# Kernel optimization log

Hardware: AMD Instinct MI355X
Metric: run time of the kernel (lower is better)

## Reference

```python
import jax, jax.numpy as jnp
import numpy as np

MAX_SCALE_MUL = float(np.log(100.0))
EPS = 1e-12

def _l2norm(t):
    # F.normalize(dim=-1): x / max(||x||_2, eps)
    n = jnp.sqrt(jnp.sum(t * t, axis=-1, keepdims=True))
    return t / jnp.maximum(n, EPS)

def setup_inputs() -> dict:
    key = jax.random.key(0)
    ks = jax.random.split(key, 6)
    B, L, C, H = 2, 2048, 1024, 16
    x = jax.random.normal(ks[0], (B, L, C), dtype=jnp.float32)
    attn_bias = jax.random.normal(ks[1], (1, 1, L, L), dtype=jnp.float32) * 0.02
    W_qkv = jax.random.normal(ks[2], (3 * C, C), dtype=jnp.float32) * (1.0 / np.sqrt(C))
    q_bias = jnp.zeros((C,), dtype=jnp.float32)
    v_bias = jnp.zeros((C,), dtype=jnp.float32)
    scale_mul_1H11 = jnp.full((1, H, 1, 1), np.log(4.0), dtype=jnp.float32)
    W_proj = jax.random.normal(ks[3], (C, C), dtype=jnp.float32) * (1.0 / np.sqrt(C))
    b_proj = jnp.zeros((C,), dtype=jnp.float32)
    return {"x": x, "attn_bias": attn_bias, "W_qkv": W_qkv, "q_bias": q_bias,
            "v_bias": v_bias, "scale_mul_1H11": scale_mul_1H11,
            "W_proj": W_proj, "b_proj": b_proj}

def reference(x, attn_bias, W_qkv, q_bias, v_bias, scale_mul_1H11, W_proj, b_proj):
    B, L, C = x.shape
    H = scale_mul_1H11.shape[1]
    D = C // H
    # qkv projection (no linear bias) + concatenated (q_bias, 0, v_bias)
    bias = jnp.concatenate([q_bias, jnp.zeros_like(q_bias), v_bias])
    pre_qkv = jnp.einsum('blc,oc->blo', x, W_qkv) + bias  # (B,L,3C)
    qkv = pre_qkv.reshape(B, L, 3, H, D).transpose(2, 0, 3, 1, 4)  # (3,B,H,L,D)
    q, k, v = qkv[0], qkv[1], qkv[2]
    # cosine attention: l2-normalize q,k; q scaled by learned per-head scale
    scale_mul = jnp.exp(jnp.minimum(scale_mul_1H11, MAX_SCALE_MUL))
    q = _l2norm(q) * scale_mul
    k = _l2norm(k)
    # slow_attn_original with scale=1 (attn_l2_norm path)
    attn = jnp.einsum('bhld,bhmd->bhlm', q, k) + attn_bias  # (B,H,L,L)
    attn = jax.nn.softmax(attn, axis=-1)
    oup = jnp.einsum('bhlm,bhmd->bhld', attn, v)  # (B,H,L,D)
    oup = oup.transpose(0, 2, 1, 3).reshape(B, L, C)
    return jnp.einsum('blc,oc->blo', oup, W_proj) + b_proj
```

## Files before the change

kernel.cpp:

```cpp
#include <hip/hip_runtime.h>

typedef short bf16x8 __attribute__((ext_vector_type(8)));
typedef short bf16x4 __attribute__((ext_vector_type(4)));
typedef unsigned short u16x8 __attribute__((ext_vector_type(8)));
typedef float f32x4 __attribute__((ext_vector_type(4)));

__device__ __forceinline__ float bf2f(unsigned short u) {
  union { unsigned int i; float f; } v; v.i = ((unsigned int)u) << 16; return v.f;
}
__device__ __forceinline__ unsigned short f2bf(float f) {
  union { float fl; unsigned int i; } v; v.fl = f;
  unsigned int r = v.i + 0x7FFFu + ((v.i >> 16) & 1u);
  return (unsigned short)(r >> 16);
}
__device__ __forceinline__ unsigned int cvt_pk_bf16(float lo, float hi) {
  unsigned int d;
  asm("v_cvt_pk_bf16_f32 %0, %1, %2" : "=v"(d) : "v"(lo), "v"(hi));
  return d;
}
__device__ __forceinline__ void gload_lds16(const void* g, void* l) {
  __builtin_amdgcn_global_load_lds(
      (const __attribute__((address_space(1))) void*)g,
      (__attribute__((address_space(3))) void*)l, 16, 0, 0);
}

__global__ __launch_bounds__(256) void cvt_bf16(const float* __restrict__ in,
                                                unsigned short* __restrict__ out, int n8) {
  int i = blockIdx.x * 256 + threadIdx.x;
  if (i >= n8) return;
  float4 a = ((const float4*)in)[2 * i];
  float4 b = ((const float4*)in)[2 * i + 1];
  u16x8 o;
  o[0] = f2bf(a.x); o[1] = f2bf(a.y); o[2] = f2bf(a.z); o[3] = f2bf(a.w);
  o[4] = f2bf(b.x); o[5] = f2bf(b.y); o[6] = f2bf(b.z); o[7] = f2bf(b.w);
  ((u16x8*)out)[i] = o;
}

template <bool F32OUT>
__global__ __launch_bounds__(256) void gemm_nt(const unsigned short* __restrict__ A,
                                               const unsigned short* __restrict__ B,
                                               void* __restrict__ Cout,
                                               const float* __restrict__ bias,
                                               int M, int N, int K) {
  __shared__ __align__(16) unsigned short a_lds[128 * 64];
  __shared__ __align__(16) unsigned short b_lds[128 * 64];
  const int t = threadIdx.x;
  const int lane = t & 63, w = t >> 6;
  const int wm = w >> 1, wn = w & 1;
  const int r16 = lane >> 4, c16 = lane & 15;
  const int m0 = blockIdx.y * 128, n0 = blockIdx.x * 128;
  f32x4 acc[4][4] = {};
  for (int k0 = 0; k0 < K; k0 += 64) {
#pragma unroll
    for (int i = 0; i < 4; ++i) {
      int s = i * 256 + t;
      int row = s >> 3, c = s & 7;
      int cs = c ^ (row & 7);
      gload_lds16(A + (size_t)(m0 + row) * K + k0 + cs * 8, (char*)a_lds + s * 16);
      gload_lds16(B + (size_t)(n0 + row) * K + k0 + cs * 8, (char*)b_lds + s * 16);
    }
    __syncthreads();
#pragma unroll
    for (int ks = 0; ks < 2; ++ks) {
      bf16x8 af[4], bfr[4];
#pragma unroll
      for (int mi = 0; mi < 4; ++mi) {
        int row = wm * 64 + mi * 16 + c16;
        int ch = (r16 + ks * 4) ^ (row & 7);
        af[mi] = *(const bf16x8*)&a_lds[row * 64 + ch * 8];
      }
#pragma unroll
      for (int ni = 0; ni < 4; ++ni) {
        int row = wn * 64 + ni * 16 + c16;
        int ch = (r16 + ks * 4) ^ (row & 7);
        bfr[ni] = *(const bf16x8*)&b_lds[row * 64 + ch * 8];
      }
#pragma unroll
      for (int mi = 0; mi < 4; ++mi)
#pragma unroll
        for (int ni = 0; ni < 4; ++ni)
          acc[mi][ni] = __builtin_amdgcn_mfma_f32_16x16x32_bf16(af[mi], bfr[ni], acc[mi][ni], 0, 0, 0);
    }
    __syncthreads();
  }
#pragma unroll
  for (int mi = 0; mi < 4; ++mi)
#pragma unroll
    for (int ni = 0; ni < 4; ++ni)
#pragma unroll
      for (int r = 0; r < 4; ++r) {
        int m = m0 + wm * 64 + mi * 16 + r16 * 4 + r;
        int n = n0 + wn * 64 + ni * 16 + c16;
        float v = acc[mi][ni][r];
        if constexpr (F32OUT) {
          ((float*)Cout)[(size_t)m * N + n] = v + bias[n];
        } else {
          ((unsigned short*)Cout)[(size_t)m * N + n] = f2bf(v);
        }
      }
}

__global__ __launch_bounds__(256) void norm_pack(const unsigned short* __restrict__ pre,
                                                 const float* __restrict__ q_bias,
                                                 const float* __restrict__ v_bias,
                                                 const float* __restrict__ scale_mul,
                                                 unsigned short* __restrict__ qo,
                                                 unsigned short* __restrict__ ko,
                                                 unsigned short* __restrict__ vto) {
  __shared__ float tl[64][65];
  const int t = threadIdx.x;
  const int li = t >> 2, dq = t & 3;
  const int tile = blockIdx.x;
  const int sl = blockIdx.y;
  const int qkv = sl >> 4, h = sl & 15;
  const int b = tile >> 5, lt = tile & 31;
  const int l = lt * 64 + li;
  const int dbase = dq * 16;
  const unsigned short* src = pre + ((size_t)b * 2048 + l) * 3072 + qkv * 1024 + h * 64 + dbase;
  float v[16];
  bf16x8 x0 = *(const bf16x8*)src;
  bf16x8 x1 = *(const bf16x8*)(src + 8);
#pragma unroll
  for (int j = 0; j < 8; ++j) {
    v[j] = bf2f((unsigned short)x0[j]);
    v[8 + j] = bf2f((unsigned short)x1[j]);
  }
  if (qkv == 0) {
#pragma unroll
    for (int j = 0; j < 16; ++j) v[j] += q_bias[h * 64 + dbase + j];
  } else if (qkv == 2) {
#pragma unroll
    for (int j = 0; j < 16; ++j) v[j] += v_bias[h * 64 + dbase + j];
  }
  if (qkv < 2) {
    float ss = 0.f;
#pragma unroll
    for (int j = 0; j < 16; ++j) ss += v[j] * v[j];
    ss += __shfl_xor(ss, 1);
    ss += __shfl_xor(ss, 2);
    float inv = 1.0f / fmaxf(sqrtf(ss), 1e-12f);
    if (qkv == 0) inv *= __expf(fminf(scale_mul[h], 4.6051701859880914f));
    u16x8 o0, o1;
#pragma unroll
    for (int j = 0; j < 8; ++j) {
      o0[j] = f2bf(v[j] * inv);
      o1[j] = f2bf(v[8 + j] * inv);
    }
    unsigned short* dst = (qkv == 0 ? qo : ko) + ((size_t)(b * 16 + h) * 2048 + l) * 64 + dbase;
    *(u16x8*)dst = o0;
    *(u16x8*)(dst + 8) = o1;
  } else {
#pragma unroll
    for (int j = 0; j < 16; ++j) tl[li][dbase + j] = v[j];
    __syncthreads();
    const int d = li;
    const int lb = dq * 16;
    u16x8 o0, o1;
#pragma unroll
    for (int j = 0; j < 8; ++j) {
      o0[j] = f2bf(tl[lb + j][d]);
      o1[j] = f2bf(tl[lb + 8 + j][d]);
    }
    unsigned short* dst = vto + ((size_t)(b * 16 + h) * 64 + d) * 2048 + lt * 64 + lb;
    *(u16x8*)dst = o0;
    *(u16x8*)(dst + 8) = o1;
  }
}

__global__ __launch_bounds__(256) void attn_fwd(const unsigned short* __restrict__ qb,
                                                const unsigned short* __restrict__ kbuf,
                                                const unsigned short* __restrict__ vtb,
                                                const unsigned short* __restrict__ biasb,
                                                const float* __restrict__ scale_mul,
                                                unsigned short* __restrict__ oup) {
  __shared__ __align__(16) unsigned short k_lds[64 * 64];
  __shared__ __align__(16) unsigned short vt_lds[64 * 64];
  __shared__ __align__(16) unsigned short b_lds[64 * 64];
  __shared__ __align__(16) unsigned short p_lds[64 * 64];
  const int t = threadIdx.x;
  const int lane = t & 63, w = t >> 6;
  const int r16 = lane >> 4, c16 = lane & 15;
  const int q0 = blockIdx.x * 64;
  const int bh = blockIdx.y;
  const int h = bh & 15;
  const size_t qk_base = (size_t)bh * 2048 * 64;
  bf16x8 aq0, aq1;
  {
    int row = q0 + w * 16 + c16;
    const unsigned short* qp = qb + qk_base + (size_t)row * 64 + r16 * 8;
    aq0 = *(const bf16x8*)qp;
    aq1 = *(const bf16x8*)(qp + 32);
  }
  const float M = __expf(fminf(scale_mul[h], 4.6051701859880914f));
  f32x4 o[4] = {};
  float lsum = 0.f;
  const int prow = w * 16 + c16;
  const int m7 = c16 & 7;
  for (int kb0 = 0; kb0 < 2048; kb0 += 64) {
#pragma unroll
    for (int i = 0; i < 2; ++i) {
      int s = i * 256 + t;
      int row = s >> 3, c = s & 7;
      int cs = c ^ (row & 7);
      gload_lds16(kbuf + qk_base + (size_t)(kb0 + row) * 64 + cs * 8, (char*)k_lds + s * 16);
      gload_lds16(vtb + qk_base + (size_t)row * 2048 + kb0 + cs * 8, (char*)vt_lds + s * 16);
      gload_lds16(biasb + (size_t)(q0 + row) * 2048 + kb0 + cs * 8, (char*)b_lds + s * 16);
    }
    __syncthreads();
    f32x4 s4[4] = {};
    __builtin_amdgcn_s_setprio(1);
#pragma unroll
    for (int ks = 0; ks < 2; ++ks) {
      bf16x8 a = ks ? aq1 : aq0;
#pragma unroll
      for (int mi = 0; mi < 4; ++mi) {
        int row = mi * 16 + c16;
        int ch = (r16 + ks * 4) ^ (row & 7);
        bf16x8 bk = *(const bf16x8*)&k_lds[row * 64 + ch * 8];
        s4[mi] = __builtin_amdgcn_mfma_f32_16x16x32_bf16(bk, a, s4[mi], 0, 0, 0);
      }
    }
    __builtin_amdgcn_s_setprio(0);
    float p[4][4];
#pragma unroll
    for (int mi = 0; mi < 4; ++mi) {
      int ch = (2 * mi + (r16 >> 1)) ^ m7;
      bf16x4 b4 = *(const bf16x4*)&b_lds[prow * 64 + ch * 8 + 4 * (r16 & 1)];
#pragma unroll
      for (int r = 0; r < 4; ++r) {
        float tv = s4[mi][r] + bf2f((unsigned short)b4[r]);
        p[mi][r] = __expf(tv - M);
      }
    }
#pragma unroll
    for (int mi = 0; mi < 4; ++mi)
      lsum += (p[mi][0] + p[mi][1]) + (p[mi][2] + p[mi][3]);
#pragma unroll
    for (int mi = 0; mi < 4; ++mi)
#pragma unroll
      for (int r2 = 0; r2 < 2; ++r2) {
        unsigned int pk = cvt_pk_bf16(p[mi][2 * r2], p[mi][2 * r2 + 1]);
        int ch = (2 * mi + (r16 >> 1)) ^ m7;
        ((unsigned int*)p_lds)[prow * 32 + ch * 4 + 2 * (r16 & 1) + r2] = pk;
      }
    __builtin_amdgcn_s_setprio(1);
#pragma unroll
    for (int ks = 0; ks < 2; ++ks) {
      int ch = (4 * ks + r16) ^ m7;
      bf16x8 ap = *(const bf16x8*)&p_lds[prow * 64 + ch * 8];
#pragma unroll
      for (int nd = 0; nd < 4; ++nd) {
        int drow = nd * 16 + c16;
        int chv = (r16 + ks * 4) ^ (drow & 7);
        bf16x8 bv = *(const bf16x8*)&vt_lds[drow * 64 + chv * 8];
        o[nd] = __builtin_amdgcn_mfma_f32_16x16x32_bf16(ap, bv, o[nd], 0, 0, 0);
      }
    }
    __builtin_amdgcn_s_setprio(0);
    __syncthreads();
  }
  lsum += __shfl_xor(lsum, 16);
  lsum += __shfl_xor(lsum, 32);
  const int b = bh >> 4;
  const int qrow_g = q0 + w * 16 + r16 * 4;
#pragma unroll
  for (int r = 0; r < 4; ++r) {
    float lr = __shfl(lsum, r16 * 4 + r);
    float inv = 1.0f / lr;
#pragma unroll
    for (int nd = 0; nd < 4; ++nd) {
      int lq = qrow_g + r;
      int d = nd * 16 + c16;
      oup[((size_t)b * 2048 + lq) * 1024 + h * 64 + d] = f2bf(o[nd][r] * inv);
    }
  }
}

extern "C" void kernel_launch(void* const* d_in, const int* in_sizes, int n_in,
                              void* d_out, int out_size, void* d_ws, size_t ws_size,
                              hipStream_t stream) {
  const float* x = (const float*)d_in[0];
  const float* attn_bias = (const float*)d_in[1];
  const float* W_qkv = (const float*)d_in[2];
  const float* q_bias = (const float*)d_in[3];
  const float* v_bias = (const float*)d_in[4];
  const float* scale_mul = (const float*)d_in[5];
  const float* W_proj = (const float*)d_in[6];
  const float* b_proj = (const float*)d_in[7];
  float* out = (float*)d_out;
  char* ws = (char*)d_ws;

  unsigned short* x_bf = (unsigned short*)(ws + 0);
  unsigned short* wqkv_bf = (unsigned short*)(ws + 8388608);
  unsigned short* wproj_bf = (unsigned short*)(ws + 14680064);
  unsigned short* bias_bf = (unsigned short*)(ws + 16777216);
  unsigned short* q_pk = (unsigned short*)(ws + 25165824);
  unsigned short* k_pk = (unsigned short*)(ws + 33554432);
  unsigned short* vt_pk = (unsigned short*)(ws + 41943040);
  unsigned short* oup_bf = (unsigned short*)(ws + 50331648);
  unsigned short* pre_qkv = (unsigned short*)(ws + 58720256);

  cvt_bf16<<<2048, 256, 0, stream>>>(x, x_bf, 524288);
  cvt_bf16<<<1536, 256, 0, stream>>>(W_qkv, wqkv_bf, 393216);
  cvt_bf16<<<512, 256, 0, stream>>>(W_proj, wproj_bf, 131072);
  cvt_bf16<<<2048, 256, 0, stream>>>(attn_bias, bias_bf, 524288);

  gemm_nt<false><<<dim3(24, 32), 256, 0, stream>>>(x_bf, wqkv_bf, (void*)pre_qkv, nullptr,
                                                   4096, 3072, 1024);
  norm_pack<<<dim3(64, 48), 256, 0, stream>>>(pre_qkv, q_bias, v_bias, scale_mul,
                                              q_pk, k_pk, vt_pk);
  attn_fwd<<<dim3(32, 32), 256, 0, stream>>>(q_pk, k_pk, vt_pk, bias_bf, scale_mul, oup_bf);
  gemm_nt<true><<<dim3(8, 32), 256, 0, stream>>>(oup_bf, wproj_bf, (void*)out, b_proj,
                                                 4096, 1024, 1024);
}
```

Measured before the change: 163.6 us.

## Read fp32 attention bias directly into registers and swizzle attention block order

Drops the separate bf16 conversion kernel for the L×L attention bias. The attention kernel now loads fp32 bias values straight from global memory into registers for each key block, instead of staging bf16 bias through LDS. It also remaps the 1D block index so blocks sharing the same bias rows and heads are spread across the XCDs/L2, and it packs the P stores into 64-bit LDS writes. The trade is one fewer launch and a bias pass saved, against twice the bias bytes read per attention block, with those reads no longer asynchronous to LDS.

```diff
diff --git a/kernel.cpp b/kernel.cpp
--- a/kernel.cpp
+++ b/kernel.cpp
@@ -1,9 +1,9 @@
 #include <hip/hip_runtime.h>
 
 typedef short bf16x8 __attribute__((ext_vector_type(8)));
-typedef short bf16x4 __attribute__((ext_vector_type(4)));
 typedef unsigned short u16x8 __attribute__((ext_vector_type(8)));
 typedef float f32x4 __attribute__((ext_vector_type(4)));
+typedef unsigned int u32x2 __attribute__((ext_vector_type(2)));
 
 __device__ __forceinline__ float bf2f(unsigned short u) {
   union { unsigned int i; float f; } v; v.i = ((unsigned int)u) << 16; return v.f;
@@ -170,18 +170,19 @@
 __global__ __launch_bounds__(256) void attn_fwd(const unsigned short* __restrict__ qb,
                                                 const unsigned short* __restrict__ kbuf,
                                                 const unsigned short* __restrict__ vtb,
-                                                const unsigned short* __restrict__ biasb,
+                                                const float* __restrict__ biasf,
                                                 const float* __restrict__ scale_mul,
                                                 unsigned short* __restrict__ oup) {
   __shared__ __align__(16) unsigned short k_lds[64 * 64];
   __shared__ __align__(16) unsigned short vt_lds[64 * 64];
-  __shared__ __align__(16) unsigned short b_lds[64 * 64];
   __shared__ __align__(16) unsigned short p_lds[64 * 64];
   const int t = threadIdx.x;
   const int lane = t & 63, w = t >> 6;
   const int r16 = lane >> 4, c16 = lane & 15;
-  const int q0 = blockIdx.x * 64;
-  const int bh = blockIdx.y;
+  const int bid = blockIdx.x;
+  const int swz = (bid & 7) * 128 + (bid >> 3);
+  const int bh = swz >> 5;
+  const int q0 = (swz & 31) * 64;
   const int h = bh & 15;
   const size_t qk_base = (size_t)bh * 2048 * 64;
   bf16x8 aq0, aq1;
@@ -196,6 +197,7 @@
   float lsum = 0.f;
   const int prow = w * 16 + c16;
   const int m7 = c16 & 7;
+  const float* bias_row = biasf + (size_t)(q0 + prow) * 2048 + r16 * 4;
   for (int kb0 = 0; kb0 < 2048; kb0 += 64) {
 #pragma unroll
     for (int i = 0; i < 2; ++i) {
@@ -204,8 +206,11 @@
       int cs = c ^ (row & 7);
       gload_lds16(kbuf + qk_base + (size_t)(kb0 + row) * 64 + cs * 8, (char*)k_lds + s * 16);
       gload_lds16(vtb + qk_base + (size_t)row * 2048 + kb0 + cs * 8, (char*)vt_lds + s * 16);
-      gload_lds16(biasb + (size_t)(q0 + row) * 2048 + kb0 + cs * 8, (char*)b_lds + s * 16);
-    }
+    }
+    float4 bias_v[4];
+#pragma unroll
+    for (int mi = 0; mi < 4; ++mi)
+      bias_v[mi] = *(const float4*)(bias_row + kb0 + mi * 16);
     __syncthreads();
     f32x4 s4[4] = {};
     __builtin_amdgcn_s_setprio(1);
@@ -223,26 +228,21 @@
     __builtin_amdgcn_s_setprio(0);
     float p[4][4];
 #pragma unroll
-    for (int mi = 0; mi < 4; ++mi) {
-      int ch = (2 * mi + (r16 >> 1)) ^ m7;
-      bf16x4 b4 = *(const bf16x4*)&b_lds[prow * 64 + ch * 8 + 4 * (r16 & 1)];
-#pragma unroll
-      for (int r = 0; r < 4; ++r) {
-        float tv = s4[mi][r] + bf2f((unsigned short)b4[r]);
-        p[mi][r] = __expf(tv - M);
-      }
-    }
+    for (int mi = 0; mi < 4; ++mi)
+#pragma unroll
+      for (int r = 0; r < 4; ++r)
+        p[mi][r] = __expf(s4[mi][r] + ((const float*)&bias_v[mi])[r] - M);
 #pragma unroll
     for (int mi = 0; mi < 4; ++mi)
       lsum += (p[mi][0] + p[mi][1]) + (p[mi][2] + p[mi][3]);
 #pragma unroll
-    for (int mi = 0; mi < 4; ++mi)
-#pragma unroll
-      for (int r2 = 0; r2 < 2; ++r2) {
-        unsigned int pk = cvt_pk_bf16(p[mi][2 * r2], p[mi][2 * r2 + 1]);
-        int ch = (2 * mi + (r16 >> 1)) ^ m7;
-        ((unsigned int*)p_lds)[prow * 32 + ch * 4 + 2 * (r16 & 1) + r2] = pk;
-      }
+    for (int mi = 0; mi < 4; ++mi) {
+      u32x2 pk2;
+      pk2[0] = cvt_pk_bf16(p[mi][0], p[mi][1]);
+      pk2[1] = cvt_pk_bf16(p[mi][2], p[mi][3]);
+      int ch = (2 * mi + (r16 >> 1)) ^ m7;
+      ((u32x2*)p_lds)[prow * 16 + ch * 2 + (r16 & 1)] = pk2;
+    }
     __builtin_amdgcn_s_setprio(1);
 #pragma unroll
     for (int ks = 0; ks < 2; ++ks) {
@@ -293,7 +293,6 @@
   unsigned short* x_bf = (unsigned short*)(ws + 0);
   unsigned short* wqkv_bf = (unsigned short*)(ws + 8388608);
   unsigned short* wproj_bf = (unsigned short*)(ws + 14680064);
-  unsigned short* bias_bf = (unsigned short*)(ws + 16777216);
   unsigned short* q_pk = (unsigned short*)(ws + 25165824);
   unsigned short* k_pk = (unsigned short*)(ws + 33554432);
   unsigned short* vt_pk = (unsigned short*)(ws + 41943040);
@@ -303,13 +302,12 @@
   cvt_bf16<<<2048, 256, 0, stream>>>(x, x_bf, 524288);
   cvt_bf16<<<1536, 256, 0, stream>>>(W_qkv, wqkv_bf, 393216);
   cvt_bf16<<<512, 256, 0, stream>>>(W_proj, wproj_bf, 131072);
-  cvt_bf16<<<2048, 256, 0, stream>>>(attn_bias, bias_bf, 524288);
 
   gemm_nt<false><<<dim3(24, 32), 256, 0, stream>>>(x_bf, wqkv_bf, (void*)pre_qkv, nullptr,
                                                    4096, 3072, 1024);
   norm_pack<<<dim3(64, 48), 256, 0, stream>>>(pre_qkv, q_bias, v_bias, scale_mul,
                                               q_pk, k_pk, vt_pk);
-  attn_fwd<<<dim3(32, 32), 256, 0, stream>>>(q_pk, k_pk, vt_pk, bias_bf, scale_mul, oup_bf);
+  attn_fwd<<<1024, 256, 0, stream>>>(q_pk, k_pk, vt_pk, attn_bias, scale_mul, oup_bf);
   gemm_nt<true><<<dim3(8, 32), 256, 0, stream>>>(oup_bf, wproj_bf, (void*)out, b_proj,
                                                  4096, 1024, 1024);
 }
```

Result: slower. 182.1 us (+11.3%).
